# Optimization experiments

Hardware: AMD Instinct MI355X
Metric: run time of the kernel (lower is better)

## Reference

```python
import jax, jax.numpy as jnp
import numpy as np

B, V, NFEAT, INTER, NHID1, NHID12, NCLASS = 131072, 8, 32, 8, 16, 8, 2


def setup_inputs() -> dict:
    key = jax.random.key(0)
    ks = jax.random.split(key, 16)
    # node feature tensor: channel 0 = node type in {0,1}, channels 1..32 = features
    types = jax.random.randint(ks[0], (B, V, 1), 0, 2).astype(jnp.float32)
    feats = jax.random.normal(ks[1], (B, V, NFEAT), dtype=jnp.float32)
    x = jnp.concatenate([types, feats], axis=-1)  # (B, V, 33)
    adj = jax.random.uniform(ks[2], (B, V, V), dtype=jnp.float32)
    edge_attr = jax.random.normal(ks[3], (B, V, V), dtype=jnp.float32)
    s = lambda k, *sh: jax.random.normal(k, sh, dtype=jnp.float32) * 0.1
    return {
        "x": x, "adj": adj, "edge_attr": edge_attr,
        "wa": s(ks[4], INTER, NFEAT), "ba": jnp.zeros((INTER,), jnp.float32),
        "wb": s(ks[5], INTER, NFEAT), "bb": jnp.zeros((INTER,), jnp.float32),
        "w1": s(ks[6], NFEAT, NHID1), "b1": jnp.zeros((NHID1,), jnp.float32),
        "w2": s(ks[7], NHID1, NHID12), "b2": jnp.zeros((NHID12,), jnp.float32),
        "wg": s(ks[8], NHID12, NHID12), "bg": jnp.zeros((NHID12,), jnp.float32),
        "wf": s(ks[9], NCLASS, NHID12), "bf": jnp.zeros((NCLASS,), jnp.float32),
    }


def _attn_pool(h, wg, bg):
    # GlobalAttentionPooling: softmax(gate_nn(h)) over nodes, weighted sum
    gate = jax.nn.softmax(jnp.einsum('bvc,oc->bvo', h, wg) + bg, axis=1)
    return jnp.sum(gate * h, axis=1)  # (B, NHID12)


def reference(x, adj, edge_attr, wa, ba, wb, bb, w1, b1, w2, b2, wg, bg, wf, bf):
    node_types = x[..., 0]           # (B, V)
    feat = x[..., 1:]                # (B, V, 32)
    # conv_b (1x1 conv == per-node linear), output layout (B, inter, V)
    Fk = jnp.einsum('bvc,oc->bov', feat, wb) + bb[None, :, None]  # (B, 8, V=8)
    S = jax.nn.softmax(jnp.matmul(Fk, Fk), axis=1)                # (B, 8, 8)
    W = adj * (S + edge_attr)                                     # (B, V, V)
    # graph conv 1: (W @ feat) @ w1 + b1, LeakyReLU(0.01)
    h = jax.nn.leaky_relu(jnp.einsum('bvw,bwc->bvc', W, feat) @ w1 + b1)
    # graph conv 2
    h = jax.nn.leaky_relu(jnp.einsum('bvw,bwc->bvc', W, h) @ w2 + b2)  # (B, V, 8)
    # per-type masked attention pooling; types fixed to {0, 1}
    pooled = []
    for t in (0.0, 1.0):
        mask = (node_types == t)[..., None].astype(h.dtype)
        pooled.append(_attn_pool(h * mask, wg, bg))
    x_pool = jnp.mean(jnp.stack(pooled, axis=1), axis=1)  # (B, NHID12)
    return x_pool @ wf.T + bf  # (B, NCLASS)
```

## Files before the change

kernel.cpp:

```cpp
#include <hip/hip_runtime.h>


#define SLOTS 16
#define NTHREADS 128

#define WBT 0
#define W1O 256
#define W2O 768
#define WGT 896
#define BBO 960
#define B1O 968
#define B2O 984
#define WFO 992
#define BFO 1008
#define NWS 1010

typedef float v2f __attribute__((ext_vector_type(2)));
typedef float4 __attribute__((aligned(4))) f4u;

__device__ __forceinline__ float grp_sum8(float x) {
    x += __shfl_xor(x, 1);
    x += __shfl_xor(x, 2);
    x += __shfl_xor(x, 4);
    return x;
}
__device__ __forceinline__ void wavefence() { __builtin_amdgcn_wave_barrier(); }
__device__ __forceinline__ v2f mkv(float a, float b) { v2f r; r.x = a; r.y = b; return r; }

__global__ void gcn_prep(const float* __restrict__ wb, const float* __restrict__ bb,
                         const float* __restrict__ w1, const float* __restrict__ b1,
                         const float* __restrict__ w2, const float* __restrict__ b2,
                         const float* __restrict__ wg, const float* __restrict__ wf,
                         const float* __restrict__ bf, float* __restrict__ ws)
{
    const int t = threadIdx.x;
    for (int i = t; i < 256; i += 256) ws[WBT + (i & 31) * 8 + (i >> 5)] = wb[i];
    for (int i = t; i < 512; i += 256) ws[W1O + i] = w1[i];
    if (t < 128) ws[W2O + t] = w2[t];
    if (t < 64)  ws[WGT + (t & 7) * 8 + (t >> 3)] = wg[t];
    if (t < 8)   ws[BBO + t] = bb[t];
    if (t < 16)  ws[B1O + t] = b1[t];
    if (t < 8)   ws[B2O + t] = b2[t];
    if (t < 16)  ws[WFO + t] = wf[t];
    if (t < 2)   ws[BFO + t] = bf[t];
}


#define KSTEP(kk, cb) { \
    const float4 qk = *(const float4*)(SB + v * 16 + ((((kk) + (v >> 1) + sl) & 3) << 2)); \
    const float f[4] = { qk.x, qk.y, qk.z, qk.w }; \
    _Pragma("unroll") \
    for (int u = 0; u < 4; ++u) { \
        const int c = (cb) + u; \
        const v2f f2 = mkv(f[u], f[u]); \
        const float4* wbc = (const float4*)(wsW + WBT + c * 8); \
        const float4 wa = wbc[0], wbq = wbc[1]; \
        Fk2[0] = __builtin_elementwise_fma(f2, mkv(wa.x,  wa.y),  Fk2[0]); \
        Fk2[1] = __builtin_elementwise_fma(f2, mkv(wa.z,  wa.w),  Fk2[1]); \
        Fk2[2] = __builtin_elementwise_fma(f2, mkv(wbq.x, wbq.y), Fk2[2]); \
        Fk2[3] = __builtin_elementwise_fma(f2, mkv(wbq.z, wbq.w), Fk2[3]); \
        const float4* w1c = (const float4*)(wsW + W1O + c * 16); \
        const float4 wc0 = w1c[0], wc1 = w1c[1], wc2 = w1c[2], wc3 = w1c[3]; \
        g12[0] = __builtin_elementwise_fma(f2, mkv(wc0.x, wc0.y), g12[0]); \
        g12[1] = __builtin_elementwise_fma(f2, mkv(wc0.z, wc0.w), g12[1]); \
        g12[2] = __builtin_elementwise_fma(f2, mkv(wc1.x, wc1.y), g12[2]); \
        g12[3] = __builtin_elementwise_fma(f2, mkv(wc1.z, wc1.w), g12[3]); \
        g12[4] = __builtin_elementwise_fma(f2, mkv(wc2.x, wc2.y), g12[4]); \
        g12[5] = __builtin_elementwise_fma(f2, mkv(wc2.z, wc2.w), g12[5]); \
        g12[6] = __builtin_elementwise_fma(f2, mkv(wc3.x, wc3.y), g12[6]); \
        g12[7] = __builtin_elementwise_fma(f2, mkv(wc3.z, wc3.w), g12[7]); \
    } }

__global__ __launch_bounds__(NTHREADS, 4)
void gcn_fused(const float* __restrict__ x,
               const float* __restrict__ adj,
               const float* __restrict__ edge,
               const float* __restrict__ wsW,
               float* __restrict__ out, int nGroups)
{
    __shared__ __align__(16) float lds[2240];

    const int tid  = threadIdx.x;
    const int slot = tid >> 3;
    const int v    = tid & 7;
    const int sl   = slot & 7;
    float* SB = &lds[(slot >> 3) * 1120 + sl * 140];
    float* A  = SB + 64;

    long long bb_ = (long long)blockIdx.x * SLOTS + slot;
    if (bb_ >= (long long)nGroups * SLOTS) bb_ = (long long)nGroups * SLOTS - 1;
    const size_t b = (size_t)bb_;

    const float* xb = x + b * 264;
    const int nb = v & 4;
    const int cl = v & 3;
    float4 xa[4];
#pragma unroll
    for (int i = 0; i < 4; ++i)
        xa[i] = *(const f4u*)(xb + (nb + i) * 33 + 1 + cl * 4);

    const float4* ar = (const float4*)(adj  + b * 64 + (size_t)v * 8);
    const float4* er = (const float4*)(edge + b * 64 + (size_t)v * 8);
    const float4 a0 = ar[0], a1 = ar[1];
    const float4 e0 = er[0], e1 = er[1];
    const float type = xb[v * 33];

#pragma unroll
    for (int i = 0; i < 4; ++i) {
        const int n = nb + i;
        *(float4*)(SB + n * 16 + (((cl + (n >> 1) + sl) & 3) << 2)) = xa[i];
    }
    float4 xc[4];
#pragma unroll
    for (int i = 0; i < 4; ++i)
        xc[i] = *(const f4u*)(xb + (nb + i) * 33 + 17 + cl * 4);
    wavefence();

    v2f Fk2[4];
    {
        const v2f* bbp = (const v2f*)&wsW[BBO];
#pragma unroll
        for (int p = 0; p < 4; ++p) Fk2[p] = bbp[p];
    }
    v2f g12[8];
#pragma unroll
    for (int p = 0; p < 8; ++p) g12[p] = mkv(0.f, 0.f);

    KSTEP(0, 0) KSTEP(1, 4) KSTEP(2, 8) KSTEP(3, 12)
    wavefence();
#pragma unroll
    for (int i = 0; i < 4; ++i) {
        const int n = nb + i;
        *(float4*)(SB + n * 16 + (((cl + (n >> 1) + sl) & 3) << 2)) = xc[i];
    }
    wavefence();
    KSTEP(0, 16) KSTEP(1, 20) KSTEP(2, 24) KSTEP(3, 28)
    wavefence();

#pragma unroll
    for (int p = 0; p < 4; ++p) {
        A[(2 * p)     * 8 + v] = Fk2[p].x;
        A[(2 * p + 1) * 8 + v] = Fk2[p].y;
    }
    {
        float4* gp = (float4*)(SB + v * 8);
        gp[0] = make_float4(g12[0].x, g12[0].y, g12[1].x, g12[1].y);
        gp[1] = make_float4(g12[2].x, g12[2].y, g12[3].x, g12[3].y);
    }
    wavefence();

    float M[8];
#pragma unroll
    for (int o = 0; o < 8; ++o) {
        const float4* fr = (const float4*)(A + o * 8);
        const float4 r0 = fr[0], r1 = fr[1];
        v2f acc = mkv(0.f, 0.f);
        acc = __builtin_elementwise_fma(mkv(r0.x, r0.y), Fk2[0], acc);
        acc = __builtin_elementwise_fma(mkv(r0.z, r0.w), Fk2[1], acc);
        acc = __builtin_elementwise_fma(mkv(r1.x, r1.y), Fk2[2], acc);
        acc = __builtin_elementwise_fma(mkv(r1.z, r1.w), Fk2[3], acc);
        M[o] = acc.x + acc.y;
    }
    wavefence();
    float mx = M[0];
#pragma unroll
    for (int o = 1; o < 8; ++o) mx = fmaxf(mx, M[o]);
    float ssum = 0.f;
#pragma unroll
    for (int o = 0; o < 8; ++o) { M[o] = __expf(M[o] - mx); ssum += M[o]; }
    const float sinv = 1.f / ssum;
#pragma unroll
    for (int o = 0; o < 8; ++o) A[o * 8 + v] = M[o] * sinv;
    wavefence();

    const float4* sr = (const float4*)(A + v * 8);
    const float4 s0 = sr[0], s1 = sr[1];
    v2f W2[4];
    W2[0] = mkv(a0.x, a0.y) * (mkv(s0.x, s0.y) + mkv(e0.x, e0.y));
    W2[1] = mkv(a0.z, a0.w) * (mkv(s0.z, s0.w) + mkv(e0.z, e0.w));
    W2[2] = mkv(a1.x, a1.y) * (mkv(s1.x, s1.y) + mkv(e1.x, e1.y));
    W2[3] = mkv(a1.z, a1.w) * (mkv(s1.z, s1.w) + mkv(e1.z, e1.w));

    v2f m1[8];
#pragma unroll
    for (int p = 0; p < 8; ++p) m1[p] = mkv(0.f, 0.f);
#pragma unroll
    for (int w = 0; w < 8; ++w) {
        const float wv = (w & 1) ? W2[w >> 1].y : W2[w >> 1].x;
        const v2f f2 = mkv(wv, wv);
        const float4* gp = (const float4*)(SB + w * 8);
        const float4 q0 = gp[0], q1 = gp[1];
        m1[0] = __builtin_elementwise_fma(f2, mkv(q0.x, q0.y), m1[0]);
        m1[1] = __builtin_elementwise_fma(f2, mkv(q0.z, q0.w), m1[1]);
        m1[2] = __builtin_elementwise_fma(f2, mkv(q1.x, q1.y), m1[2]);
        m1[3] = __builtin_elementwise_fma(f2, mkv(q1.z, q1.w), m1[3]);
    }
    wavefence();
    {
        float4* gp = (float4*)(SB + v * 8);
        gp[0] = make_float4(g12[4].x, g12[4].y, g12[5].x, g12[5].y);
        gp[1] = make_float4(g12[6].x, g12[6].y, g12[7].x, g12[7].y);
    }
    wavefence();
#pragma unroll
    for (int w = 0; w < 8; ++w) {
        const float wv = (w & 1) ? W2[w >> 1].y : W2[w >> 1].x;
        const v2f f2 = mkv(wv, wv);
        const float4* gp = (const float4*)(SB + w * 8);
        const float4 q0 = gp[0], q1 = gp[1];
        m1[4] = __builtin_elementwise_fma(f2, mkv(q0.x, q0.y), m1[4]);
        m1[5] = __builtin_elementwise_fma(f2, mkv(q0.z, q0.w), m1[5]);
        m1[6] = __builtin_elementwise_fma(f2, mkv(q1.x, q1.y), m1[6]);
        m1[7] = __builtin_elementwise_fma(f2, mkv(q1.z, q1.w), m1[7]);
    }
    v2f h[8];
    {
        const v2f* b1p = (const v2f*)&wsW[B1O];
        const v2f k01 = mkv(0.01f, 0.01f);
#pragma unroll
        for (int p = 0; p < 8; ++p) {
            const v2f t = m1[p] + b1p[p];
            h[p] = __builtin_elementwise_max(t, t * k01);
        }
    }

    v2f g22[4];
#pragma unroll
    for (int p = 0; p < 4; ++p) g22[p] = mkv(0.f, 0.f);
#pragma unroll
    for (int j = 0; j < 16; ++j) {
        const float hv = (j & 1) ? h[j >> 1].y : h[j >> 1].x;
        const v2f f2 = mkv(hv, hv);
        const float4* w2r = (const float4*)(wsW + W2O + j * 8);
        const float4 r0 = w2r[0], r1 = w2r[1];
        g22[0] = __builtin_elementwise_fma(f2, mkv(r0.x, r0.y), g22[0]);
        g22[1] = __builtin_elementwise_fma(f2, mkv(r0.z, r0.w), g22[1]);
        g22[2] = __builtin_elementwise_fma(f2, mkv(r1.x, r1.y), g22[2]);
        g22[3] = __builtin_elementwise_fma(f2, mkv(r1.z, r1.w), g22[3]);
    }
    wavefence();
    {
        float4* gp = (float4*)(SB + v * 8);
        gp[0] = make_float4(g22[0].x, g22[0].y, g22[1].x, g22[1].y);
        gp[1] = make_float4(g22[2].x, g22[2].y, g22[3].x, g22[3].y);
    }
    wavefence();

    v2f m2[4];
#pragma unroll
    for (int p = 0; p < 4; ++p) m2[p] = mkv(0.f, 0.f);
#pragma unroll
    for (int w = 0; w < 8; ++w) {
        const float wv = (w & 1) ? W2[w >> 1].y : W2[w >> 1].x;
        const v2f f2 = mkv(wv, wv);
        const float4* gp = (const float4*)(SB + w * 8);
        const float4 q0 = gp[0], q1 = gp[1];
        m2[0] = __builtin_elementwise_fma(f2, mkv(q0.x, q0.y), m2[0]);
        m2[1] = __builtin_elementwise_fma(f2, mkv(q0.z, q0.w), m2[1]);
        m2[2] = __builtin_elementwise_fma(f2, mkv(q1.x, q1.y), m2[2]);
        m2[3] = __builtin_elementwise_fma(f2, mkv(q1.z, q1.w), m2[3]);
    }
    v2f h2[4];
    {
        const v2f* b2p = (const v2f*)&wsW[B2O];
        const v2f k01 = mkv(0.01f, 0.01f);
#pragma unroll
        for (int p = 0; p < 4; ++p) {
            const v2f t = m2[p] + b2p[p];
            h2[p] = __builtin_elementwise_max(t, t * k01);
        }
    }

    v2f Y2[4];
#pragma unroll
    for (int p = 0; p < 4; ++p) Y2[p] = mkv(0.f, 0.f);
#pragma unroll
    for (int n = 0; n < 8; ++n) {
        const float hv = (n & 1) ? h2[n >> 1].y : h2[n >> 1].x;
        const v2f f2 = mkv(hv, hv);
        const float4* wgr = (const float4*)(wsW + WGT + n * 8);
        const float4 r0 = wgr[0], r1 = wgr[1];
        Y2[0] = __builtin_elementwise_fma(f2, mkv(r0.x, r0.y), Y2[0]);
        Y2[1] = __builtin_elementwise_fma(f2, mkv(r0.z, r0.w), Y2[1]);
        Y2[2] = __builtin_elementwise_fma(f2, mkv(r1.x, r1.y), Y2[2]);
        Y2[3] = __builtin_elementwise_fma(f2, mkv(r1.z, r1.w), Y2[3]);
    }
    wavefence();
    {
        float4* pp = (float4*)(SB + v * 16);
        pp[0] = make_float4(Y2[0].x, h2[0].x, Y2[0].y, h2[0].y);
        pp[1] = make_float4(Y2[1].x, h2[1].x, Y2[1].y, h2[1].y);
        pp[2] = make_float4(Y2[2].x, h2[2].x, Y2[2].y, h2[2].y);
        pp[3] = make_float4(Y2[3].x, h2[3].x, Y2[3].y, h2[3].y);
        SB[128 + v] = type;
    }
    wavefence();

    const int o = v;
    float yc[8], hc[8], ty[8];
#pragma unroll
    for (int vp = 0; vp < 8; ++vp) {
        const float2 q = *(const float2*)(SB + vp * 16 + o * 2);
        yc[vp] = q.x;
        hc[vp] = q.y;
        ty[vp] = SB[128 + vp];
    }
    float xp = 0.f;
#pragma unroll
    for (int t = 0; t < 2; ++t) {
        const float tv = (float)t;
        float l[8];
        float lmx = -1e30f;
#pragma unroll
        for (int vp = 0; vp < 8; ++vp) {
            l[vp] = (ty[vp] == tv) ? yc[vp] : 0.f;
            lmx = fmaxf(lmx, l[vp]);
        }
        float esum = 0.f, num = 0.f;
#pragma unroll
        for (int vp = 0; vp < 8; ++vp) {
            const float e = __expf(l[vp] - lmx);
            esum += e;
            num  += (ty[vp] == tv) ? e * hc[vp] : 0.f;
        }
        xp += 0.5f * num / esum;
    }

    const float y0 = grp_sum8(xp * wsW[WFO + o]);
    const float y1 = grp_sum8(xp * wsW[WFO + 8 + o]);
    if (v == 0) {
        float2* op = (float2*)(out + b * 2);
        *op = make_float2(y0 + wsW[BFO], y1 + wsW[BFO + 1]);
    }
}

extern "C" void kernel_launch(void* const* d_in, const int* in_sizes, int n_in,
                              void* d_out, int out_size, void* d_ws, size_t ws_size,
                              hipStream_t stream) {
    const float* x    = (const float*)d_in[0];
    const float* adj  = (const float*)d_in[1];
    const float* edge = (const float*)d_in[2];
    const float* wb   = (const float*)d_in[5];
    const float* bb   = (const float*)d_in[6];
    const float* w1   = (const float*)d_in[7];
    const float* b1   = (const float*)d_in[8];
    const float* w2   = (const float*)d_in[9];
    const float* b2   = (const float*)d_in[10];
    const float* wg   = (const float*)d_in[11];
    const float* wf   = (const float*)d_in[13];
    const float* bf   = (const float*)d_in[14];
    float* out = (float*)d_out;
    float* ws  = (float*)d_ws;

    const int Btot    = in_sizes[0] / 264;
    const int nGroups = (Btot + SLOTS - 1) / SLOTS;

    gcn_prep<<<1, 256, 0, stream>>>(wb, bb, w1, b1, w2, b2, wg, wf, bf, ws);
    gcn_fused<<<nGroups, NTHREADS, 0, stream>>>(x, adj, edge, ws, out, nGroups);
}
```

Baseline: 275.2 us.

## Drop weight-prep kernel, read raw weights directly, and double block size

```diff
diff --git a/kernel.cpp b/kernel.cpp
--- a/kernel.cpp
+++ b/kernel.cpp
@@ -1,19 +1,8 @@
 #include <hip/hip_runtime.h>
 
 
-#define SLOTS 16
-#define NTHREADS 128
-
-#define WBT 0
-#define W1O 256
-#define W2O 768
-#define WGT 896
-#define BBO 960
-#define B1O 968
-#define B2O 984
-#define WFO 992
-#define BFO 1008
-#define NWS 1010
+#define SLOTS 32
+#define NTHREADS 256
 
 typedef float v2f __attribute__((ext_vector_type(2)));
 typedef float4 __attribute__((aligned(4))) f4u;
@@ -27,58 +16,37 @@
 __device__ __forceinline__ void wavefence() { __builtin_amdgcn_wave_barrier(); }
 __device__ __forceinline__ v2f mkv(float a, float b) { v2f r; r.x = a; r.y = b; return r; }
 
-__global__ void gcn_prep(const float* __restrict__ wb, const float* __restrict__ bb,
-                         const float* __restrict__ w1, const float* __restrict__ b1,
-                         const float* __restrict__ w2, const float* __restrict__ b2,
-                         const float* __restrict__ wg, const float* __restrict__ wf,
-                         const float* __restrict__ bf, float* __restrict__ ws)
-{
-    const int t = threadIdx.x;
-    for (int i = t; i < 256; i += 256) ws[WBT + (i & 31) * 8 + (i >> 5)] = wb[i];
-    for (int i = t; i < 512; i += 256) ws[W1O + i] = w1[i];
-    if (t < 128) ws[W2O + t] = w2[t];
-    if (t < 64)  ws[WGT + (t & 7) * 8 + (t >> 3)] = wg[t];
-    if (t < 8)   ws[BBO + t] = bb[t];
-    if (t < 16)  ws[B1O + t] = b1[t];
-    if (t < 8)   ws[B2O + t] = b2[t];
-    if (t < 16)  ws[WFO + t] = wf[t];
-    if (t < 2)   ws[BFO + t] = bf[t];
-}
-
 
 #define KSTEP(kk, cb) { \
     const float4 qk = *(const float4*)(SB + v * 16 + ((((kk) + (v >> 1) + sl) & 3) << 2)); \
-    const float f[4] = { qk.x, qk.y, qk.z, qk.w }; \
+    const v2f fA = mkv(qk.x, qk.y), fB = mkv(qk.z, qk.w); \
+    _Pragma("unroll") \
+    for (int o = 0; o < 8; ++o) { \
+        Fko[o] = __builtin_elementwise_fma(fA, *(const v2f*)(wb + o * 32 + (cb)),     Fko[o]); \
+        Fko[o] = __builtin_elementwise_fma(fB, *(const v2f*)(wb + o * 32 + (cb) + 2), Fko[o]); \
+    } \
+    const float fu[4] = { qk.x, qk.y, qk.z, qk.w }; \
     _Pragma("unroll") \
     for (int u = 0; u < 4; ++u) { \
         const int c = (cb) + u; \
-        const v2f f2 = mkv(f[u], f[u]); \
-        const float4* wbc = (const float4*)(wsW + WBT + c * 8); \
-        const float4 wa = wbc[0], wbq = wbc[1]; \
-        Fk2[0] = __builtin_elementwise_fma(f2, mkv(wa.x,  wa.y),  Fk2[0]); \
-        Fk2[1] = __builtin_elementwise_fma(f2, mkv(wa.z,  wa.w),  Fk2[1]); \
-        Fk2[2] = __builtin_elementwise_fma(f2, mkv(wbq.x, wbq.y), Fk2[2]); \
-        Fk2[3] = __builtin_elementwise_fma(f2, mkv(wbq.z, wbq.w), Fk2[3]); \
-        const float4* w1c = (const float4*)(wsW + W1O + c * 16); \
-        const float4 wc0 = w1c[0], wc1 = w1c[1], wc2 = w1c[2], wc3 = w1c[3]; \
-        g12[0] = __builtin_elementwise_fma(f2, mkv(wc0.x, wc0.y), g12[0]); \
-        g12[1] = __builtin_elementwise_fma(f2, mkv(wc0.z, wc0.w), g12[1]); \
-        g12[2] = __builtin_elementwise_fma(f2, mkv(wc1.x, wc1.y), g12[2]); \
-        g12[3] = __builtin_elementwise_fma(f2, mkv(wc1.z, wc1.w), g12[3]); \
-        g12[4] = __builtin_elementwise_fma(f2, mkv(wc2.x, wc2.y), g12[4]); \
-        g12[5] = __builtin_elementwise_fma(f2, mkv(wc2.z, wc2.w), g12[5]); \
-        g12[6] = __builtin_elementwise_fma(f2, mkv(wc3.x, wc3.y), g12[6]); \
-        g12[7] = __builtin_elementwise_fma(f2, mkv(wc3.z, wc3.w), g12[7]); \
+        const v2f f2 = mkv(fu[u], fu[u]); \
+        _Pragma("unroll") \
+        for (int p = 0; p < 8; ++p) \
+            g12[p] = __builtin_elementwise_fma(f2, *(const v2f*)(w1 + c * 16 + 2 * p), g12[p]); \
     } }
 
 __global__ __launch_bounds__(NTHREADS, 4)
 void gcn_fused(const float* __restrict__ x,
                const float* __restrict__ adj,
                const float* __restrict__ edge,
-               const float* __restrict__ wsW,
+               const float* __restrict__ wb, const float* __restrict__ bb,
+               const float* __restrict__ w1, const float* __restrict__ b1,
+               const float* __restrict__ w2, const float* __restrict__ b2,
+               const float* __restrict__ wg,
+               const float* __restrict__ wf, const float* __restrict__ bf,
                float* __restrict__ out, int nGroups)
 {
-    __shared__ __align__(16) float lds[2240];
+    __shared__ __align__(16) float lds[4480];
 
     const int tid  = threadIdx.x;
     const int slot = tid >> 3;
@@ -116,12 +84,9 @@
         xc[i] = *(const f4u*)(xb + (nb + i) * 33 + 17 + cl * 4);
     wavefence();
 
-    v2f Fk2[4];
-    {
-        const v2f* bbp = (const v2f*)&wsW[BBO];
-#pragma unroll
-        for (int p = 0; p < 4; ++p) Fk2[p] = bbp[p];
-    }
+    v2f Fko[8];
+#pragma unroll
+    for (int o = 0; o < 8; ++o) Fko[o] = mkv(0.f, 0.f);
     v2f g12[8];
 #pragma unroll
     for (int p = 0; p < 8; ++p) g12[p] = mkv(0.f, 0.f);
@@ -137,17 +102,22 @@
     KSTEP(0, 16) KSTEP(1, 20) KSTEP(2, 24) KSTEP(3, 28)
     wavefence();
 
-#pragma unroll
-    for (int p = 0; p < 4; ++p) {
-        A[(2 * p)     * 8 + v] = Fk2[p].x;
-        A[(2 * p + 1) * 8 + v] = Fk2[p].y;
-    }
+    float Fks[8];
+#pragma unroll
+    for (int o = 0; o < 8; ++o) Fks[o] = Fko[o].x + Fko[o].y + bb[o];
+
+#pragma unroll
+    for (int o = 0; o < 8; ++o) A[o * 8 + v] = Fks[o];
     {
         float4* gp = (float4*)(SB + v * 8);
         gp[0] = make_float4(g12[0].x, g12[0].y, g12[1].x, g12[1].y);
         gp[1] = make_float4(g12[2].x, g12[2].y, g12[3].x, g12[3].y);
     }
     wavefence();
+
+    v2f Fk2[4];
+#pragma unroll
+    for (int p = 0; p < 4; ++p) Fk2[p] = mkv(Fks[2 * p], Fks[2 * p + 1]);
 
     float M[8];
 #pragma unroll
@@ -215,11 +185,10 @@
     }
     v2f h[8];
     {
-        const v2f* b1p = (const v2f*)&wsW[B1O];
         const v2f k01 = mkv(0.01f, 0.01f);
 #pragma unroll
         for (int p = 0; p < 8; ++p) {
-            const v2f t = m1[p] + b1p[p];
+            const v2f t = m1[p] + *(const v2f*)(b1 + 2 * p);
             h[p] = __builtin_elementwise_max(t, t * k01);
         }
     }
@@ -231,12 +200,9 @@
     for (int j = 0; j < 16; ++j) {
         const float hv = (j & 1) ? h[j >> 1].y : h[j >> 1].x;
         const v2f f2 = mkv(hv, hv);
-        const float4* w2r = (const float4*)(wsW + W2O + j * 8);
-        const float4 r0 = w2r[0], r1 = w2r[1];
-        g22[0] = __builtin_elementwise_fma(f2, mkv(r0.x, r0.y), g22[0]);
-        g22[1] = __builtin_elementwise_fma(f2, mkv(r0.z, r0.w), g22[1]);
-        g22[2] = __builtin_elementwise_fma(f2, mkv(r1.x, r1.y), g22[2]);
-        g22[3] = __builtin_elementwise_fma(f2, mkv(r1.z, r1.w), g22[3]);
+#pragma unroll
+        for (int p = 0; p < 4; ++p)
+            g22[p] = __builtin_elementwise_fma(f2, *(const v2f*)(w2 + j * 8 + 2 * p), g22[p]);
     }
     wavefence();
     {
@@ -262,36 +228,30 @@
     }
     v2f h2[4];
     {
-        const v2f* b2p = (const v2f*)&wsW[B2O];
         const v2f k01 = mkv(0.01f, 0.01f);
 #pragma unroll
         for (int p = 0; p < 4; ++p) {
-            const v2f t = m2[p] + b2p[p];
+            const v2f t = m2[p] + *(const v2f*)(b2 + 2 * p);
             h2[p] = __builtin_elementwise_max(t, t * k01);
         }
     }
 
-    v2f Y2[4];
-#pragma unroll
-    for (int p = 0; p < 4; ++p) Y2[p] = mkv(0.f, 0.f);
-#pragma unroll
-    for (int n = 0; n < 8; ++n) {
-        const float hv = (n & 1) ? h2[n >> 1].y : h2[n >> 1].x;
-        const v2f f2 = mkv(hv, hv);
-        const float4* wgr = (const float4*)(wsW + WGT + n * 8);
-        const float4 r0 = wgr[0], r1 = wgr[1];
-        Y2[0] = __builtin_elementwise_fma(f2, mkv(r0.x, r0.y), Y2[0]);
-        Y2[1] = __builtin_elementwise_fma(f2, mkv(r0.z, r0.w), Y2[1]);
-        Y2[2] = __builtin_elementwise_fma(f2, mkv(r1.x, r1.y), Y2[2]);
-        Y2[3] = __builtin_elementwise_fma(f2, mkv(r1.z, r1.w), Y2[3]);
+    float Ys[8];
+#pragma unroll
+    for (int o = 0; o < 8; ++o) {
+        v2f acc = mkv(0.f, 0.f);
+#pragma unroll
+        for (int p = 0; p < 4; ++p)
+            acc = __builtin_elementwise_fma(h2[p], *(const v2f*)(wg + o * 8 + 2 * p), acc);
+        Ys[o] = acc.x + acc.y;
     }
     wavefence();
     {
         float4* pp = (float4*)(SB + v * 16);
-        pp[0] = make_float4(Y2[0].x, h2[0].x, Y2[0].y, h2[0].y);
-        pp[1] = make_float4(Y2[1].x, h2[1].x, Y2[1].y, h2[1].y);
-        pp[2] = make_float4(Y2[2].x, h2[2].x, Y2[2].y, h2[2].y);
-        pp[3] = make_float4(Y2[3].x, h2[3].x, Y2[3].y, h2[3].y);
+        pp[0] = make_float4(Ys[0], h2[0].x, Ys[1], h2[0].y);
+        pp[1] = make_float4(Ys[2], h2[1].x, Ys[3], h2[1].y);
+        pp[2] = make_float4(Ys[4], h2[2].x, Ys[5], h2[2].y);
+        pp[3] = make_float4(Ys[6], h2[3].x, Ys[7], h2[3].y);
         SB[128 + v] = type;
     }
     wavefence();
@@ -326,11 +286,11 @@
         xp += 0.5f * num / esum;
     }
 
-    const float y0 = grp_sum8(xp * wsW[WFO + o]);
-    const float y1 = grp_sum8(xp * wsW[WFO + 8 + o]);
+    const float y0 = grp_sum8(xp * wf[0 * 8 + o]);
+    const float y1 = grp_sum8(xp * wf[1 * 8 + o]);
     if (v == 0) {
         float2* op = (float2*)(out + b * 2);
-        *op = make_float2(y0 + wsW[BFO], y1 + wsW[BFO + 1]);
+        *op = make_float2(y0 + bf[0], y1 + bf[1]);
     }
 }
 
@@ -350,11 +310,10 @@
     const float* wf   = (const float*)d_in[13];
     const float* bf   = (const float*)d_in[14];
     float* out = (float*)d_out;
-    float* ws  = (float*)d_ws;
 
     const int Btot    = in_sizes[0] / 264;
     const int nGroups = (Btot + SLOTS - 1) / SLOTS;
 
-    gcn_prep<<<1, 256, 0, stream>>>(wb, bb, w1, b1, w2, b2, wg, wf, bf, ws);
-    gcn_fused<<<nGroups, NTHREADS, 0, stream>>>(x, adj, edge, ws, out, nGroups);
+    gcn_fused<<<nGroups, NTHREADS, 0, stream>>>(x, adj, edge, wb, bb, w1, b1,
+                                                w2, b2, wg, wf, bf, out, nGroups);
 }
```

New measurement: 273.2 us. No clear change (-0.7%).
